# Kernel tuning notes

Measured on AMD Instinct MI355X. Metric: run time of the kernel, lower is better.

## Reference

```python
import jax, jax.numpy as jnp
import numpy as np

N = 6144      # number of pedestrians
HID = 256     # hidden_dim
OUT = 32      # out_dim
NTOP = 4      # n nearest neighbours
EMB = OUT // NTOP  # per-neighbour embedding dim = 8


def setup_inputs() -> dict:
    key = jax.random.key(0)
    ks = jax.random.split(key, 12)
    r = lambda k, shp, s=1.0: (jax.random.normal(k, shp, dtype=jnp.float32) * s)
    return {
        "obs1": r(ks[0], (N, 2)),
        "obs2": r(ks[1], (N, 2)),
        "h": r(ks[2], (N, HID), 0.1),
        "c": r(ks[3], (N, HID), 0.1),
        "W_emb": r(ks[4], (4, EMB), 0.3),
        "b_emb": r(ks[5], (EMB,), 0.1),
        "W_ih": r(ks[6], (4 * HID, OUT), 0.1),
        "b_ih": r(ks[7], (4 * HID,), 0.1),
        "W_hh": r(ks[8], (4 * HID, HID), 0.1),
        "b_hh": r(ks[9], (4 * HID,), 0.1),
        "W_pool": r(ks[10], (OUT, HID), 0.1),
        "b_pool": r(ks[11], (OUT,), 0.1),
    }


def reference(obs1, obs2, h, c, W_emb, b_emb, W_ih, b_ih, W_hh, b_hh, W_pool, b_pool):
    n = obs2.shape[0]
    vel = obs2 - obs1                                   # [N,2]
    # rel_position[i, j] = obs2[j] - obs2[i]
    diff = obs2[None, :, :] - obs2[:, None, :]          # [N,N,2]
    dist = jnp.linalg.norm(diff, axis=-1)               # [N,N]
    # exclude self (torch code drops the diagonal before topk)
    dist = jnp.where(jnp.eye(n, dtype=bool), jnp.inf, dist)
    _, idx = jax.lax.top_k(-dist, NTOP)                 # [N,NTOP] indices of nearest
    nearest_pos = jnp.take_along_axis(diff, idx[:, :, None], axis=1)  # [N,NTOP,2]
    # rel_direction[i, j] = vel[j] - vel[i]
    nearest_vel = vel[idx] - vel[:, None, :]            # [N,NTOP,2]
    feat = jnp.concatenate([nearest_pos, nearest_vel], axis=-1)       # [N,NTOP,4]
    # Linear(4, EMB) + ReLU, then flatten neighbours -> [N, OUT]
    emb = jax.nn.relu(feat @ W_emb + b_emb).reshape(n, -1)
    # LSTMCell (PyTorch gate order: i, f, g, o)
    gates = emb @ W_ih.T + b_ih + h @ W_hh.T + b_hh     # [N,4*HID]
    gi, gf, gg, go = jnp.split(gates, 4, axis=-1)
    c_new = jax.nn.sigmoid(gf) * c + jax.nn.sigmoid(gi) * jnp.tanh(gg)
    h_new = jax.nn.sigmoid(go) * jnp.tanh(c_new)
    out = h_new @ W_pool.T + b_pool                     # [N,OUT]
    return out
```

## Files before the change

### kernel.cpp

```cpp
#include <hip/hip_runtime.h>
#include <math.h>

typedef unsigned short u16;
typedef unsigned long long u64;
typedef __attribute__((ext_vector_type(8))) short bf16x8;
typedef __attribute__((ext_vector_type(4))) float f32x4;

__device__ __forceinline__ float sigf(float x)  { return 1.0f / (1.0f + __expf(-x)); }
__device__ __forceinline__ float tanhf_(float x){ float e = __expf(2.0f * x); return 1.0f - 2.0f / (e + 1.0f); }
__device__ __forceinline__ u16 f2bf(float f) {
    unsigned x = __float_as_uint(f);
    return (u16)((x + 0x7fffu + ((x >> 16) & 1u)) >> 16);
}

#define INSU(KEY) do {                                                              \
    u64 _k = (KEY);                                                                 \
    k3 = (_k < k3) ? _k : k3;                                                       \
    { bool _c = k3 < k2; u64 _lo = _c ? k3 : k2, _hi = _c ? k2 : k3; k2 = _lo; k3 = _hi; } \
    { bool _c = k2 < k1; u64 _lo = _c ? k2 : k1, _hi = _c ? k1 : k2; k1 = _lo; k2 = _hi; } \
    { bool _c = k1 < k0; u64 _lo = _c ? k1 : k0, _hi = _c ? k0 : k1; k0 = _lo; k1 = _hi; } \
} while (0)

#define INS4(D, J) do {                                                              \
    float _d = (D); int _j = (J);                                                    \
    if (_d < bd3 || (_d == bd3 && _j < bj3)) {                                       \
        bd3 = _d; bj3 = _j;                                                          \
        if (bd3 < bd2 || (bd3 == bd2 && bj3 < bj2)) {                                \
            float _t = bd2; bd2 = bd3; bd3 = _t; int _u = bj2; bj2 = bj3; bj3 = _u; }\
        if (bd2 < bd1 || (bd2 == bd1 && bj2 < bj1)) {                                \
            float _t = bd1; bd1 = bd2; bd2 = _t; int _u = bj1; bj1 = bj2; bj2 = _u; }\
        if (bd1 < bd0 || (bd1 == bd0 && bj1 < bj0)) {                                \
            float _t = bd0; bd0 = bd1; bd1 = _t; int _u = bj0; bj0 = bj1; bj1 = _u; }\
    } } while (0)

__global__ void diag_kernel(float* out, int code, int out_size) {
    if (out_size > 0) out[0] = (float)code * 1.0e8f;
}

__device__ __forceinline__ void prep_item(
    int id, const float* Wih, const float* Whh, const float* Wp,
    u16* Wgf, u16* Wpf)
{
    if (id < 36864) {
        int gt = id / 576, rem = id - gt * 576;
        int kt = rem >> 6, ln = rem & 63;
        int g  = gt * 16 + (ln & 15);
        int k  = kt * 32 + (ln >> 4) * 8;
        u16* dst = Wgf + (size_t)id * 8;
        #pragma unroll
        for (int j = 0; j < 8; j++) {
            int kk = k + j;
            float v = (kk < 32) ? Wih[(size_t)g * 32 + kk]
                                : Whh[(size_t)g * 256 + (kk - 32)];
            dst[j] = f2bf(v);
        }
    } else if (id < 37888) {
        int id2 = id - 36864;
        int pt = id2 >> 9, rem = id2 & 511;
        int kt = rem >> 6, ln = rem & 63;
        int o  = pt * 16 + (ln & 15);
        int k  = kt * 32 + (ln >> 4) * 8;
        u16* dst = Wpf + (size_t)id2 * 8;
        #pragma unroll
        for (int j = 0; j < 8; j++)
            dst[j] = f2bf(Wp[(size_t)o * 256 + k + j]);
    }
}

__global__ __launch_bounds__(256) void knn_prep_kernel(
    const float* __restrict__ obs1, const float* __restrict__ obs2,
    const float* __restrict__ Wemb, const float* __restrict__ bemb,
    const float* __restrict__ Wih,  const float* __restrict__ Whh,
    const float* __restrict__ Wp,
    u16* __restrict__ Wgf, u16* __restrict__ Wpf,
    int n, int knn_blocks, float* __restrict__ out)
{
    const int t = threadIdx.x;

    if (blockIdx.x >= knn_blocks) {
        int id = (blockIdx.x - knn_blocks) * 256 + t;
        prep_item(id, Wih, Whh, Wp, Wgf, Wpf);
        return;
    }

    const int lane = t & 63;
    const int wv   = t >> 6;
    const int i    = blockIdx.x * 4 + wv;
    if (i >= n) return;

    const float2* o2 = (const float2*)obs2;
    const float2 pi = o2[i];

    u64 k0 = ~0ull, k1 = ~0ull, k2 = ~0ull, k3 = ~0ull;

    int j = lane;
    for (; j + 192 < n; j += 256) {
        float2 p0 = o2[j], p1 = o2[j + 64], p2 = o2[j + 128], p3 = o2[j + 192];
        float dx, dy, d2; u64 key;
        dx = p0.x - pi.x; dy = p0.y - pi.y;
        d2 = __fadd_rn(__fmul_rn(dx, dx), __fmul_rn(dy, dy));
        key = (((u64)__float_as_uint(d2)) << 24) | (unsigned)j;
        key = (j == i) ? ~0ull : key;                         INSU(key);
        dx = p1.x - pi.x; dy = p1.y - pi.y;
        d2 = __fadd_rn(__fmul_rn(dx, dx), __fmul_rn(dy, dy));
        key = (((u64)__float_as_uint(d2)) << 24) | (unsigned)(j + 64);
        key = (j + 64 == i) ? ~0ull : key;                    INSU(key);
        dx = p2.x - pi.x; dy = p2.y - pi.y;
        d2 = __fadd_rn(__fmul_rn(dx, dx), __fmul_rn(dy, dy));
        key = (((u64)__float_as_uint(d2)) << 24) | (unsigned)(j + 128);
        key = (j + 128 == i) ? ~0ull : key;                   INSU(key);
        dx = p3.x - pi.x; dy = p3.y - pi.y;
        d2 = __fadd_rn(__fmul_rn(dx, dx), __fmul_rn(dy, dy));
        key = (((u64)__float_as_uint(d2)) << 24) | (unsigned)(j + 192);
        key = (j + 192 == i) ? ~0ull : key;                   INSU(key);
    }
    for (; j < n; j += 64) {
        float2 pj = o2[j];
        float dx = pj.x - pi.x, dy = pj.y - pi.y;
        float d2 = __fadd_rn(__fmul_rn(dx, dx), __fmul_rn(dy, dy));
        u64 key = (((u64)__float_as_uint(d2)) << 24) | (unsigned)j;
        key = (j == i) ? ~0ull : key;
        INSU(key);
    }

    #pragma unroll
    for (int m = 1; m < 64; m <<= 1) {
        u64 o0 = __shfl_xor(k0, m), o1 = __shfl_xor(k1, m);
        u64 o2_ = __shfl_xor(k2, m), o3 = __shfl_xor(k3, m);
        INSU(o0); INSU(o1); INSU(o2_); INSU(o3);
    }

    if (lane < 4) {
        u64 kq = (lane == 0) ? k0 : (lane == 1) ? k1 : (lane == 2) ? k2 : k3;
        int jn = (int)(kq & 0xFFFFFF);
        if (jn < 0 || jn >= n) jn = 0;
        float pix = pi.x, piy = pi.y;
        float pjx = obs2[2 * jn], pjy = obs2[2 * jn + 1];
        float px = pjx - pix, py = pjy - piy;
        float vix = pix - obs1[2 * i];
        float viy = piy - obs1[2 * i + 1];
        float vx = (pjx - obs1[2 * jn])     - vix;
        float vy = (pjy - obs1[2 * jn + 1]) - viy;
        float* dst = out + (size_t)i * 32 + lane * 8;
        #pragma unroll
        for (int e = 0; e < 8; e++) {
            float a = px * Wemb[e]      + py * Wemb[8 + e]
                    + vx * Wemb[16 + e] + vy * Wemb[24 + e]
                    + bemb[e];
            dst[e] = fmaxf(a, 0.0f);
        }
    }
}

__global__ __launch_bounds__(512) void lstm_kernel(
    const float* __restrict__ h,   const float* __restrict__ c,
    const u16*  __restrict__ Wgf,  const float* __restrict__ bih,
    const float* __restrict__ bhh,
    const u16*  __restrict__ Wpf,  const float* __restrict__ bp,
    int n, float* __restrict__ out)
{
    __shared__ __align__(16) char lds[17920];
    u16* sXb = (u16*)lds;
    u16* sHb = (u16*)(lds + 9472);

    const int t    = threadIdx.x;
    const int i0   = blockIdx.x * 12;
    const int lane = t & 63;
    const int wv   = t >> 6;
    const int fm   = lane & 15;
    const int fq   = lane >> 4;

    {
        int r = t >> 5, e = t & 31;
        int row = i0 + r;
        float v = (r < 12 && row < n) ? out[(size_t)row * 32 + e] : 0.0f;
        sXb[r * 296 + e] = f2bf(v);
    }
    #pragma unroll
    for (int f = t; f < 16 * 64; f += 512) {
        int r = f >> 6, k4 = f & 63;
        int row = i0 + r;
        float4 hv = (r < 12 && row < n) ? ((const float4*)h)[(size_t)row * 64 + k4]
                                        : make_float4(0.f, 0.f, 0.f, 0.f);
        u16* d = &sXb[r * 296 + 32 + k4 * 4];
        d[0] = f2bf(hv.x); d[1] = f2bf(hv.y); d[2] = f2bf(hv.z); d[3] = f2bf(hv.w);
    }
    __syncthreads();

    bf16x8 afr[9];
    #pragma unroll
    for (int kt = 0; kt < 9; kt++)
        afr[kt] = *(const bf16x8*)&sXb[fm * 296 + kt * 32 + fq * 8];

    #pragma unroll
    for (int ut2 = 0; ut2 < 2; ut2++) {
        const int ut = wv + ut2 * 8;
        const int u  = ut * 16 + fm;

        f32x4 acc[4];
        #pragma unroll
        for (int jg = 0; jg < 4; jg++) acc[jg] = (f32x4){0.f, 0.f, 0.f, 0.f};

        #pragma unroll
        for (int jg = 0; jg < 4; jg++) {
            const int gt = jg * 16 + ut;
            const u16* wbase = Wgf + ((size_t)gt * 9) * 512 + lane * 8;
            #pragma unroll
            for (int kt = 0; kt < 9; kt++) {
                bf16x8 bfr = *(const bf16x8*)(wbase + kt * 512);
                acc[jg] = __builtin_amdgcn_mfma_f32_16x16x32_bf16(afr[kt], bfr, acc[jg], 0, 0, 0);
            }
        }

        float b0 = bih[u]       + bhh[u];
        float b1 = bih[u + 256] + bhh[u + 256];
        float b2 = bih[u + 512] + bhh[u + 512];
        float b3 = bih[u + 768] + bhh[u + 768];

        #pragma unroll
        for (int r_ = 0; r_ < 4; r_++) {
            int rl = fq * 4 + r_;
            int row = i0 + rl;
            bool valid = (rl < 12) && (row < n);
            float cin = valid ? c[(size_t)row * 256 + u] : 0.0f;
            float gi = acc[0][r_] + b0;
            float gf = acc[1][r_] + b1;
            float gg = acc[2][r_] + b2;
            float go = acc[3][r_] + b3;
            float cn = sigf(gf) * cin + sigf(gi) * tanhf_(gg);
            float hn = sigf(go) * tanhf_(cn);
            sHb[rl * 264 + u] = valid ? f2bf(hn) : (u16)0;
        }
    }
    __syncthreads();

    if (wv < 2) {
        bf16x8 ah[8];
        #pragma unroll
        for (int kt = 0; kt < 8; kt++)
            ah[kt] = *(const bf16x8*)&sHb[fm * 264 + kt * 32 + fq * 8];
        const u16* wbase = Wpf + ((size_t)wv * 8) * 512 + lane * 8;
        f32x4 acc = {0.f, 0.f, 0.f, 0.f};
        #pragma unroll
        for (int kt = 0; kt < 8; kt++) {
            bf16x8 bfr = *(const bf16x8*)(wbase + kt * 512);
            acc = __builtin_amdgcn_mfma_f32_16x16x32_bf16(ah[kt], bfr, acc, 0, 0, 0);
        }
        float bias = bp[wv * 16 + fm];
        #pragma unroll
        for (int r_ = 0; r_ < 4; r_++) {
            int rl = fq * 4 + r_;
            int row = i0 + rl;
            if (rl < 12 && row < n) out[(size_t)row * 32 + wv * 16 + fm] = acc[r_] + bias;
        }
    }
}

__global__ __launch_bounds__(256) void nnlstm_fallback(
    const float* __restrict__ obs1, const float* __restrict__ obs2,
    const float* __restrict__ h,    const float* __restrict__ c,
    const float* __restrict__ Wemb, const float* __restrict__ bemb,
    const float* __restrict__ Wih,  const float* __restrict__ bih,
    const float* __restrict__ Whh,  const float* __restrict__ bhh,
    const float* __restrict__ Wp,   const float* __restrict__ bp,
    int n, float* __restrict__ out)
{
    __shared__ float sMd[16][64];
    __shared__ int   sMj[16][64];
    __shared__ float sX[16][292];
    __shared__ float sH[16][264];

    const int t   = threadIdx.x;
    const int sub = t & 15;
    const int ii  = t >> 4;
    const int i0  = blockIdx.x * 16;
    const int i   = i0 + ii;

    for (int v = t; v < 16 * 256; v += 256) {
        int r = v >> 8, k = v & 255;
        int row = i0 + r;
        sX[r][32 + k] = (row < n) ? h[(size_t)row * 256 + k] : 0.0f;
    }

    float bd0 = 1e30f, bd1 = 1e30f, bd2 = 1e30f, bd3 = 1e30f;
    int   bj0 = 0x7fffffff, bj1 = 0x7fffffff, bj2 = 0x7fffffff, bj3 = 0x7fffffff;

    if (i < n) {
        const float pix = obs2[2 * i];
        const float piy = obs2[2 * i + 1];
        for (int j = sub; j < n; j += 16) {
            float dx = obs2[2 * j]     - pix;
            float dy = obs2[2 * j + 1] - piy;
            float d2 = __fadd_rn(__fmul_rn(dx, dx), __fmul_rn(dy, dy));
            float dist = __fsqrt_rn(d2);
            if (j == i) continue;
            INS4(dist, j);
        }
    }
    sMd[ii][sub * 4 + 0] = bd0;  sMj[ii][sub * 4 + 0] = bj0;
    sMd[ii][sub * 4 + 1] = bd1;  sMj[ii][sub * 4 + 1] = bj1;
    sMd[ii][sub * 4 + 2] = bd2;  sMj[ii][sub * 4 + 2] = bj2;
    sMd[ii][sub * 4 + 3] = bd3;  sMj[ii][sub * 4 + 3] = bj3;
    __syncthreads();

    if (t < 16) {
        const int r = t;
        const int irow = i0 + r;
        float bd0 = 1e30f, bd1 = 1e30f, bd2 = 1e30f, bd3 = 1e30f;
        int   bj0 = 0x7fffffff, bj1 = 0x7fffffff, bj2 = 0x7fffffff, bj3 = 0x7fffffff;
        for (int q = 0; q < 64; q++) { INS4(sMd[r][q], sMj[r][q]); }

        if (irow < n) {
            float pix = obs2[2 * irow], piy = obs2[2 * irow + 1];
            float vix = pix - obs1[2 * irow];
            float viy = piy - obs1[2 * irow + 1];
            #pragma unroll
            for (int q2 = 0; q2 < 4; q2++) {
                int jn = (q2 == 0) ? bj0 : (q2 == 1) ? bj1 : (q2 == 2) ? bj2 : bj3;
                if (jn < 0 || jn >= n) jn = 0;
                float pjx = obs2[2 * jn], pjy = obs2[2 * jn + 1];
                float px = pjx - pix, py = pjy - piy;
                float vx = (pjx - obs1[2 * jn])     - vix;
                float vy = (pjy - obs1[2 * jn + 1]) - viy;
                #pragma unroll
                for (int e = 0; e < 8; e++) {
                    float a = px * Wemb[e]      + py * Wemb[8 + e]
                            + vx * Wemb[16 + e] + vy * Wemb[24 + e]
                            + bemb[e];
                    sX[r][q2 * 8 + e] = fmaxf(a, 0.0f);
                }
            }
        } else {
            for (int e = 0; e < 32; e++) sX[r][e] = 0.0f;
        }
    }
    __syncthreads();

    const int uu = t;
    float acc[4][16];
    #pragma unroll
    for (int j = 0; j < 4; j++) {
        float b = bih[uu + 256 * j] + bhh[uu + 256 * j];
        #pragma unroll
        for (int r = 0; r < 16; r++) acc[j][r] = b;
    }

    for (int kc = 0; kc < 288; kc++) {
        float w[4];
        #pragma unroll
        for (int j = 0; j < 4; j++) {
            int g = uu + 256 * j;
            w[j] = (kc < 32) ? Wih[(size_t)g * 32 + kc]
                             : Whh[(size_t)g * 256 + (kc - 32)];
        }
        #pragma unroll
        for (int r = 0; r < 16; r++) {
            float x = sX[r][kc];
            #pragma unroll
            for (int j = 0; j < 4; j++) acc[j][r] += w[j] * x;
        }
    }

    for (int r = 0; r < 16; r++) {
        int row = i0 + r;
        float cin = (row < n) ? c[(size_t)row * 256 + uu] : 0.0f;
        float cn = sigf(acc[1][r]) * cin + sigf(acc[0][r]) * tanhf(acc[2][r]);
        float hn = sigf(acc[3][r]) * tanhf(cn);
        sH[r][uu] = hn;
    }
    __syncthreads();

    for (int v = t; v < 16 * 32; v += 256) {
        int r = v >> 5, o = v & 31;
        int row = i0 + r;
        if (row >= n) continue;
        float a = bp[o];
        for (int kc = 0; kc < 256; kc++)
            a += Wp[(size_t)o * 256 + kc] * sH[r][kc];
        out[(size_t)row * 32 + o] = a;
    }
}

extern "C" void kernel_launch(void* const* d_in, const int* in_sizes, int n_in,
                              void* d_out, int out_size, void* d_ws, size_t ws_size,
                              hipStream_t stream) {
    float* out = (float*)d_out;

    int code = 0, n = 0;
    if (n_in != 12) code = 1;
    else {
        n = in_sizes[1] / 2;
        if (n <= 4 || in_sizes[1] != 2 * n)          code = 2;
        else if (in_sizes[0]  != 2 * n)              code = 3;
        else if (in_sizes[2]  != 256 * n)            code = 4;
        else if (in_sizes[3]  != 256 * n)            code = 5;
        else if (in_sizes[4]  != 32 || in_sizes[5] != 8)        code = 6;
        else if (in_sizes[6]  != 32768 || in_sizes[7] != 1024)  code = 7;
        else if (in_sizes[8]  != 262144 || in_sizes[9] != 1024) code = 8;
        else if (in_sizes[10] != 8192 || in_sizes[11] != 32)    code = 9;
        else if (out_size != 32 * n)                 code = 10;
    }
    if (code != 0) {
        diag_kernel<<<1, 1, 0, stream>>>(out, code, out_size);
        return;
    }

    const float* obs1   = (const float*)d_in[0];
    const float* obs2   = (const float*)d_in[1];
    const float* h      = (const float*)d_in[2];
    const float* c      = (const float*)d_in[3];
    const float* W_emb  = (const float*)d_in[4];
    const float* b_emb  = (const float*)d_in[5];
    const float* W_ih   = (const float*)d_in[6];
    const float* b_ih   = (const float*)d_in[7];
    const float* W_hh   = (const float*)d_in[8];
    const float* b_hh   = (const float*)d_in[9];
    const float* W_pool = (const float*)d_in[10];
    const float* b_pool = (const float*)d_in[11];

    const size_t wgf_bytes = (size_t)36864 * 8 * sizeof(u16);
    const size_t wpf_bytes = (size_t)1024 * 8 * sizeof(u16);

    if (ws_size >= wgf_bytes + wpf_bytes && n <= (1 << 24)) {
        u16* Wgf = (u16*)d_ws;
        u16* Wpf = (u16*)((char*)d_ws + wgf_bytes);
        int knn_blocks = (n + 3) / 4;
        knn_prep_kernel<<<knn_blocks + 148, 256, 0, stream>>>(
            obs1, obs2, W_emb, b_emb, W_ih, W_hh, W_pool, Wgf, Wpf,
            n, knn_blocks, out);
        lstm_kernel<<<(n + 11) / 12, 512, 0, stream>>>(
            h, c, Wgf, b_ih, b_hh, Wpf, b_pool, n, out);
    } else {
        nnlstm_fallback<<<(n + 15) / 16, 256, 0, stream>>>(
            obs1, obs2, h, c, W_emb, b_emb, W_ih, b_ih, W_hh, b_hh,
            W_pool, b_pool, n, out);
    }
}
```

Before: 142.9 us.

## Two-pass KNN: float-only threshold pass, then filtered keyed top-4 selection

Replaces the single pass that ran 64-bit key insertion sorts for every candidate with two passes. The first pass keeps four independent float-only top-4 lists per lane, merges them with min/max networks and a wave butterfly to get the 4th-smallest distance as a threshold. The second pass recomputes distances and does the 64-bit key insert only for candidates at or below that threshold, so most candidates skip it. The cost is reading obs2 and computing distances twice, plus possible lane divergence in the filtered branch.

```diff
diff --git a/kernel.cpp b/kernel.cpp
--- a/kernel.cpp
+++ b/kernel.cpp
@@ -19,6 +19,24 @@
     { bool _c = k3 < k2; u64 _lo = _c ? k3 : k2, _hi = _c ? k2 : k3; k2 = _lo; k3 = _hi; } \
     { bool _c = k2 < k1; u64 _lo = _c ? k2 : k1, _hi = _c ? k1 : k2; k1 = _lo; k2 = _hi; } \
     { bool _c = k1 < k0; u64 _lo = _c ? k1 : k0, _hi = _c ? k0 : k1; k0 = _lo; k1 = _hi; } \
+} while (0)
+
+#define INSF(T0,T1,T2,T3,D) do {                                                    \
+    float _ma = fmaxf((D),(T0)); (T0) = fminf((D),(T0));                            \
+    float _mb = fmaxf(_ma,(T1)); (T1) = fminf(_ma,(T1));                            \
+    float _mc = fmaxf(_mb,(T2)); (T2) = fminf(_mb,(T2));                            \
+    (T3) = fminf(_mc,(T3));                                                         \
+} while (0)
+
+#define MRG4(X0,X1,X2,X3,Y0,Y1,Y2,Y3) do {                                          \
+    float _q0 = fminf((X0),(Y3));                                                   \
+    float _q1 = fminf((X1),(Y2));                                                   \
+    float _q2 = fminf((X2),(Y1));                                                   \
+    float _q3 = fminf((X3),(Y0));                                                   \
+    float _l0 = fminf(_q0,_q2), _h0 = fmaxf(_q0,_q2);                               \
+    float _l1 = fminf(_q1,_q3), _h1 = fmaxf(_q1,_q3);                               \
+    (X0) = fminf(_l0,_l1); (X1) = fmaxf(_l0,_l1);                                   \
+    (X2) = fminf(_h0,_h1); (X3) = fmaxf(_h0,_h1);                                   \
 } while (0)
 
 #define INS4(D, J) do {                                                              \
@@ -88,39 +106,96 @@
     const int i    = blockIdx.x * 4 + wv;
     if (i >= n) return;
 
+    const float FINF = __int_as_float(0x7f800000);
     const float2* o2 = (const float2*)obs2;
     const float2 pi = o2[i];
 
-    u64 k0 = ~0ull, k1 = ~0ull, k2 = ~0ull, k3 = ~0ull;
+    float A0=FINF, A1=FINF, A2=FINF, A3=FINF;
+    float B0=FINF, B1=FINF, B2=FINF, B3=FINF;
+    float C0=FINF, C1=FINF, C2=FINF, C3=FINF;
+    float D0=FINF, D1=FINF, D2=FINF, D3=FINF;
 
     int j = lane;
     for (; j + 192 < n; j += 256) {
         float2 p0 = o2[j], p1 = o2[j + 64], p2 = o2[j + 128], p3 = o2[j + 192];
-        float dx, dy, d2; u64 key;
+        float dx, dy, d2;
         dx = p0.x - pi.x; dy = p0.y - pi.y;
         d2 = __fadd_rn(__fmul_rn(dx, dx), __fmul_rn(dy, dy));
-        key = (((u64)__float_as_uint(d2)) << 24) | (unsigned)j;
-        key = (j == i) ? ~0ull : key;                         INSU(key);
+        d2 = (j == i) ? FINF : d2;               INSF(A0, A1, A2, A3, d2);
         dx = p1.x - pi.x; dy = p1.y - pi.y;
         d2 = __fadd_rn(__fmul_rn(dx, dx), __fmul_rn(dy, dy));
-        key = (((u64)__float_as_uint(d2)) << 24) | (unsigned)(j + 64);
-        key = (j + 64 == i) ? ~0ull : key;                    INSU(key);
+        d2 = (j + 64 == i) ? FINF : d2;          INSF(B0, B1, B2, B3, d2);
         dx = p2.x - pi.x; dy = p2.y - pi.y;
         d2 = __fadd_rn(__fmul_rn(dx, dx), __fmul_rn(dy, dy));
-        key = (((u64)__float_as_uint(d2)) << 24) | (unsigned)(j + 128);
-        key = (j + 128 == i) ? ~0ull : key;                   INSU(key);
+        d2 = (j + 128 == i) ? FINF : d2;         INSF(C0, C1, C2, C3, d2);
         dx = p3.x - pi.x; dy = p3.y - pi.y;
         d2 = __fadd_rn(__fmul_rn(dx, dx), __fmul_rn(dy, dy));
-        key = (((u64)__float_as_uint(d2)) << 24) | (unsigned)(j + 192);
-        key = (j + 192 == i) ? ~0ull : key;                   INSU(key);
+        d2 = (j + 192 == i) ? FINF : d2;         INSF(D0, D1, D2, D3, d2);
     }
     for (; j < n; j += 64) {
         float2 pj = o2[j];
         float dx = pj.x - pi.x, dy = pj.y - pi.y;
         float d2 = __fadd_rn(__fmul_rn(dx, dx), __fmul_rn(dy, dy));
-        u64 key = (((u64)__float_as_uint(d2)) << 24) | (unsigned)j;
-        key = (j == i) ? ~0ull : key;
-        INSU(key);
+        d2 = (j == i) ? FINF : d2;
+        INSF(A0, A1, A2, A3, d2);
+    }
+
+    MRG4(A0, A1, A2, A3, B0, B1, B2, B3);
+    MRG4(C0, C1, C2, C3, D0, D1, D2, D3);
+    MRG4(A0, A1, A2, A3, C0, C1, C2, C3);
+
+    #pragma unroll
+    for (int m = 1; m < 64; m <<= 1) {
+        float y0 = __shfl_xor(A0, m), y1 = __shfl_xor(A1, m);
+        float y2 = __shfl_xor(A2, m), y3 = __shfl_xor(A3, m);
+        MRG4(A0, A1, A2, A3, y0, y1, y2, y3);
+    }
+    const float thr = A3;
+
+    u64 k0 = ~0ull, k1 = ~0ull, k2 = ~0ull, k3 = ~0ull;
+
+    j = lane;
+    for (; j + 192 < n; j += 256) {
+        float2 p0 = o2[j], p1 = o2[j + 64], p2 = o2[j + 128], p3 = o2[j + 192];
+        float dx, dy, d2;
+        dx = p0.x - pi.x; dy = p0.y - pi.y;
+        d2 = __fadd_rn(__fmul_rn(dx, dx), __fmul_rn(dy, dy));
+        if (d2 <= thr) {
+            u64 key = (((u64)__float_as_uint(d2)) << 24) | (unsigned)j;
+            key = (j == i) ? ~0ull : key;
+            INSU(key);
+        }
+        dx = p1.x - pi.x; dy = p1.y - pi.y;
+        d2 = __fadd_rn(__fmul_rn(dx, dx), __fmul_rn(dy, dy));
+        if (d2 <= thr) {
+            u64 key = (((u64)__float_as_uint(d2)) << 24) | (unsigned)(j + 64);
+            key = (j + 64 == i) ? ~0ull : key;
+            INSU(key);
+        }
+        dx = p2.x - pi.x; dy = p2.y - pi.y;
+        d2 = __fadd_rn(__fmul_rn(dx, dx), __fmul_rn(dy, dy));
+        if (d2 <= thr) {
+            u64 key = (((u64)__float_as_uint(d2)) << 24) | (unsigned)(j + 128);
+            key = (j + 128 == i) ? ~0ull : key;
+            INSU(key);
+        }
+        dx = p3.x - pi.x; dy = p3.y - pi.y;
+        d2 = __fadd_rn(__fmul_rn(dx, dx), __fmul_rn(dy, dy));
+        if (d2 <= thr) {
+            u64 key = (((u64)__float_as_uint(d2)) << 24) | (unsigned)(j + 192);
+            key = (j + 192 == i) ? ~0ull : key;
+            INSU(key);
+        }
+    }
+    for (; j < n; j += 64) {
+        float2 pj = o2[j];
+        float dx = pj.x - pi.x, dy = pj.y - pi.y;
+        float d2 = __fadd_rn(__fmul_rn(dx, dx), __fmul_rn(dy, dy));
+        if (d2 <= thr) {
+            u64 key = (((u64)__float_as_uint(d2)) << 24) | (unsigned)j;
+            key = (j == i) ? ~0ull : key;
+            INSU(key);
+        }
     }
 
     #pragma unroll
```

After: 145.7 us. No clear change (+1.9%).

## Two-pass kNN with float threshold pass and LDS-staged positions

Applied to the files above, without the earlier changes.

Splits the nearest-neighbour search into two passes. The first keeps four independent float-only top-4 lists per lane, using min/max networks, and merges them across the wave to get the 4th-smallest distance as a threshold. The second pass does the 64-bit key insertion only for candidates at or below that threshold. For n <= 6144 all positions are also staged in shared memory per block, so both passes read LDS instead of global memory. This trades a second distance sweep and a per-block LDS fill for avoiding the costly 64-bit sorted insert on nearly every candidate.

```diff
diff --git a/kernel.cpp b/kernel.cpp
--- a/kernel.cpp
+++ b/kernel.cpp
@@ -19,6 +19,24 @@
     { bool _c = k3 < k2; u64 _lo = _c ? k3 : k2, _hi = _c ? k2 : k3; k2 = _lo; k3 = _hi; } \
     { bool _c = k2 < k1; u64 _lo = _c ? k2 : k1, _hi = _c ? k1 : k2; k1 = _lo; k2 = _hi; } \
     { bool _c = k1 < k0; u64 _lo = _c ? k1 : k0, _hi = _c ? k0 : k1; k0 = _lo; k1 = _hi; } \
+} while (0)
+
+#define INSF(T0,T1,T2,T3,D) do {                                                    \
+    float _ma = fmaxf((D),(T0)); (T0) = fminf((D),(T0));                            \
+    float _mb = fmaxf(_ma,(T1)); (T1) = fminf(_ma,(T1));                            \
+    float _mc = fmaxf(_mb,(T2)); (T2) = fminf(_mb,(T2));                            \
+    (T3) = fminf(_mc,(T3));                                                         \
+} while (0)
+
+#define MRG4(X0,X1,X2,X3,Y0,Y1,Y2,Y3) do {                                          \
+    float _q0 = fminf((X0),(Y3));                                                   \
+    float _q1 = fminf((X1),(Y2));                                                   \
+    float _q2 = fminf((X2),(Y1));                                                   \
+    float _q3 = fminf((X3),(Y0));                                                   \
+    float _l0 = fminf(_q0,_q2), _h0 = fmaxf(_q0,_q2);                               \
+    float _l1 = fminf(_q1,_q3), _h1 = fmaxf(_q1,_q3);                               \
+    (X0) = fminf(_l0,_l1); (X1) = fmaxf(_l0,_l1);                                   \
+    (X2) = fminf(_h0,_h1); (X3) = fmaxf(_h0,_h1);                                   \
 } while (0)
 
 #define INS4(D, J) do {                                                              \
@@ -67,6 +85,7 @@
     }
 }
 
+template<bool USE_LDS>
 __global__ __launch_bounds__(256) void knn_prep_kernel(
     const float* __restrict__ obs1, const float* __restrict__ obs2,
     const float* __restrict__ Wemb, const float* __restrict__ bemb,
@@ -75,6 +94,9 @@
     u16* __restrict__ Wgf, u16* __restrict__ Wpf,
     int n, int knn_blocks, float* __restrict__ out)
 {
+    extern __shared__ __align__(16) char smem[];
+    float2* sP = (float2*)smem;
+
     const int t = threadIdx.x;
 
     if (blockIdx.x >= knn_blocks) {
@@ -86,42 +108,120 @@
     const int lane = t & 63;
     const int wv   = t >> 6;
     const int i    = blockIdx.x * 4 + wv;
+
+    const float2* o2 = (const float2*)obs2;
+
+    if (USE_LDS) {
+        const float4* o4 = (const float4*)obs2;
+        float4* s4 = (float4*)smem;
+        const int n2 = n >> 1;
+        for (int idx = t; idx < n2; idx += 256) s4[idx] = o4[idx];
+        if ((n & 1) && t == 0) sP[n - 1] = o2[n - 1];
+        __syncthreads();
+    }
+
     if (i >= n) return;
 
-    const float2* o2 = (const float2*)obs2;
+    const float FINF = __int_as_float(0x7f800000);
     const float2 pi = o2[i];
 
+    float A0=FINF, A1=FINF, A2=FINF, A3=FINF;
+    float B0=FINF, B1=FINF, B2=FINF, B3=FINF;
+    float C0=FINF, C1=FINF, C2=FINF, C3=FINF;
+    float D0=FINF, D1=FINF, D2=FINF, D3=FINF;
+
+#define P1LOOP(ARR) do {                                                            \
+    int j = lane;                                                                   \
+    for (; j + 192 < n; j += 256) {                                                 \
+        float2 p0 = (ARR)[j], p1 = (ARR)[j + 64];                                   \
+        float2 p2 = (ARR)[j + 128], p3 = (ARR)[j + 192];                            \
+        float dx, dy, d2;                                                           \
+        dx = p0.x - pi.x; dy = p0.y - pi.y;                                         \
+        d2 = __fadd_rn(__fmul_rn(dx, dx), __fmul_rn(dy, dy));                       \
+        d2 = (j == i) ? FINF : d2;               INSF(A0, A1, A2, A3, d2);          \
+        dx = p1.x - pi.x; dy = p1.y - pi.y;                                         \
+        d2 = __fadd_rn(__fmul_rn(dx, dx), __fmul_rn(dy, dy));                       \
+        d2 = (j + 64 == i) ? FINF : d2;          INSF(B0, B1, B2, B3, d2);          \
+        dx = p2.x - pi.x; dy = p2.y - pi.y;                                         \
+        d2 = __fadd_rn(__fmul_rn(dx, dx), __fmul_rn(dy, dy));                       \
+        d2 = (j + 128 == i) ? FINF : d2;         INSF(C0, C1, C2, C3, d2);          \
+        dx = p3.x - pi.x; dy = p3.y - pi.y;                                         \
+        d2 = __fadd_rn(__fmul_rn(dx, dx), __fmul_rn(dy, dy));                       \
+        d2 = (j + 192 == i) ? FINF : d2;         INSF(D0, D1, D2, D3, d2);          \
+    }                                                                               \
+    for (; j < n; j += 64) {                                                        \
+        float2 pj = (ARR)[j];                                                       \
+        float dx = pj.x - pi.x, dy = pj.y - pi.y;                                   \
+        float d2 = __fadd_rn(__fmul_rn(dx, dx), __fmul_rn(dy, dy));                 \
+        d2 = (j == i) ? FINF : d2;                                                  \
+        INSF(A0, A1, A2, A3, d2);                                                   \
+    }                                                                               \
+} while (0)
+
+    if (USE_LDS) P1LOOP(sP); else P1LOOP(o2);
+
+    MRG4(A0, A1, A2, A3, B0, B1, B2, B3);
+    MRG4(C0, C1, C2, C3, D0, D1, D2, D3);
+    MRG4(A0, A1, A2, A3, C0, C1, C2, C3);
+
+    #pragma unroll
+    for (int m = 1; m < 64; m <<= 1) {
+        float y0 = __shfl_xor(A0, m), y1 = __shfl_xor(A1, m);
+        float y2 = __shfl_xor(A2, m), y3 = __shfl_xor(A3, m);
+        MRG4(A0, A1, A2, A3, y0, y1, y2, y3);
+    }
+    const float thr = A3;
+
     u64 k0 = ~0ull, k1 = ~0ull, k2 = ~0ull, k3 = ~0ull;
 
-    int j = lane;
-    for (; j + 192 < n; j += 256) {
-        float2 p0 = o2[j], p1 = o2[j + 64], p2 = o2[j + 128], p3 = o2[j + 192];
-        float dx, dy, d2; u64 key;
-        dx = p0.x - pi.x; dy = p0.y - pi.y;
-        d2 = __fadd_rn(__fmul_rn(dx, dx), __fmul_rn(dy, dy));
-        key = (((u64)__float_as_uint(d2)) << 24) | (unsigned)j;
-        key = (j == i) ? ~0ull : key;                         INSU(key);
-        dx = p1.x - pi.x; dy = p1.y - pi.y;
-        d2 = __fadd_rn(__fmul_rn(dx, dx), __fmul_rn(dy, dy));
-        key = (((u64)__float_as_uint(d2)) << 24) | (unsigned)(j + 64);
-        key = (j + 64 == i) ? ~0ull : key;                    INSU(key);
-        dx = p2.x - pi.x; dy = p2.y - pi.y;
-        d2 = __fadd_rn(__fmul_rn(dx, dx), __fmul_rn(dy, dy));
-        key = (((u64)__float_as_uint(d2)) << 24) | (unsigned)(j + 128);
-        key = (j + 128 == i) ? ~0ull : key;                   INSU(key);
-        dx = p3.x - pi.x; dy = p3.y - pi.y;
-        d2 = __fadd_rn(__fmul_rn(dx, dx), __fmul_rn(dy, dy));
-        key = (((u64)__float_as_uint(d2)) << 24) | (unsigned)(j + 192);
-        key = (j + 192 == i) ? ~0ull : key;                   INSU(key);
-    }
-    for (; j < n; j += 64) {
-        float2 pj = o2[j];
-        float dx = pj.x - pi.x, dy = pj.y - pi.y;
-        float d2 = __fadd_rn(__fmul_rn(dx, dx), __fmul_rn(dy, dy));
-        u64 key = (((u64)__float_as_uint(d2)) << 24) | (unsigned)j;
-        key = (j == i) ? ~0ull : key;
-        INSU(key);
-    }
+#define P2LOOP(ARR) do {                                                            \
+    int j = lane;                                                                   \
+    for (; j + 192 < n; j += 256) {                                                 \
+        float2 p0 = (ARR)[j], p1 = (ARR)[j + 64];                                   \
+        float2 p2 = (ARR)[j + 128], p3 = (ARR)[j + 192];                            \
+        float dx, dy, d2;                                                           \
+        dx = p0.x - pi.x; dy = p0.y - pi.y;                                         \
+        d2 = __fadd_rn(__fmul_rn(dx, dx), __fmul_rn(dy, dy));                       \
+        if (d2 <= thr) {                                                            \
+            u64 key = (((u64)__float_as_uint(d2)) << 24) | (unsigned)j;             \
+            key = (j == i) ? ~0ull : key;                                           \
+            INSU(key);                                                              \
+        }                                                                           \
+        dx = p1.x - pi.x; dy = p1.y - pi.y;                                         \
+        d2 = __fadd_rn(__fmul_rn(dx, dx), __fmul_rn(dy, dy));                       \
+        if (d2 <= thr) {                                                            \
+            u64 key = (((u64)__float_as_uint(d2)) << 24) | (unsigned)(j + 64);      \
+            key = (j + 64 == i) ? ~0ull : key;                                      \
+            INSU(key);                                                              \
+        }                                                                           \
+        dx = p2.x - pi.x; dy = p2.y - pi.y;                                         \
+        d2 = __fadd_rn(__fmul_rn(dx, dx), __fmul_rn(dy, dy));                       \
+        if (d2 <= thr) {                                                            \
+            u64 key = (((u64)__float_as_uint(d2)) << 24) | (unsigned)(j + 128);     \
+            key = (j + 128 == i) ? ~0ull : key;                                     \
+            INSU(key);                                                              \
+        }                                                                           \
+        dx = p3.x - pi.x; dy = p3.y - pi.y;                                         \
+        d2 = __fadd_rn(__fmul_rn(dx, dx), __fmul_rn(dy, dy));                       \
+        if (d2 <= thr) {                                                            \
+            u64 key = (((u64)__float_as_uint(d2)) << 24) | (unsigned)(j + 192);     \
+            key = (j + 192 == i) ? ~0ull : key;                                     \
+            INSU(key);                                                              \
+        }                                                                           \
+    }                                                                               \
+    for (; j < n; j += 64) {                                                        \
+        float2 pj = (ARR)[j];                                                       \
+        float dx = pj.x - pi.x, dy = pj.y - pi.y;                                   \
+        float d2 = __fadd_rn(__fmul_rn(dx, dx), __fmul_rn(dy, dy));                 \
+        if (d2 <= thr) {                                                            \
+            u64 key = (((u64)__float_as_uint(d2)) << 24) | (unsigned)j;             \
+            key = (j == i) ? ~0ull : key;                                           \
+            INSU(key);                                                              \
+        }                                                                           \
+    }                                                                               \
+} while (0)
+
+    if (USE_LDS) P2LOOP(sP); else P2LOOP(o2);
 
     #pragma unroll
     for (int m = 1; m < 64; m <<= 1) {
@@ -425,9 +525,16 @@
         u16* Wgf = (u16*)d_ws;
         u16* Wpf = (u16*)((char*)d_ws + wgf_bytes);
         int knn_blocks = (n + 3) / 4;
-        knn_prep_kernel<<<knn_blocks + 148, 256, 0, stream>>>(
-            obs1, obs2, W_emb, b_emb, W_ih, W_hh, W_pool, Wgf, Wpf,
-            n, knn_blocks, out);
+        if (n <= 6144) {
+            size_t shmem = (size_t)n * sizeof(float2);
+            knn_prep_kernel<true><<<knn_blocks + 148, 256, shmem, stream>>>(
+                obs1, obs2, W_emb, b_emb, W_ih, W_hh, W_pool, Wgf, Wpf,
+                n, knn_blocks, out);
+        } else {
+            knn_prep_kernel<false><<<knn_blocks + 148, 256, 0, stream>>>(
+                obs1, obs2, W_emb, b_emb, W_ih, W_hh, W_pool, Wgf, Wpf,
+                n, knn_blocks, out);
+        }
         lstm_kernel<<<(n + 11) / 12, 512, 0, stream>>>(
             h, c, Wgf, b_ih, b_hh, Wpf, b_pool, n, out);
     } else {
```

After: 142.9 us. No clear change (-0.0%).

## Two-pass KNN: cheap min-distance threshold pass, then filtered top-4 insertion

Applied to the files above, without the earlier changes.

The KNN search now runs a first pass that keeps only per-lane minimum distances, merges them across the wavefront with a bitonic-style 4-way merge, and takes the 4th smallest of the lane minima as a threshold. A second pass recomputes distances and only does the costly 64-bit sorted insertion for candidates at or under that threshold. This cuts the comparator-network work per candidate at the cost of reading obs2 twice. The weight prep also switches to float4 loads, and launch bounds gain a min-blocks hint.

```diff
diff --git a/kernel.cpp b/kernel.cpp
--- a/kernel.cpp
+++ b/kernel.cpp
@@ -19,6 +19,17 @@
     { bool _c = k3 < k2; u64 _lo = _c ? k3 : k2, _hi = _c ? k2 : k3; k2 = _lo; k3 = _hi; } \
     { bool _c = k2 < k1; u64 _lo = _c ? k2 : k1, _hi = _c ? k1 : k2; k1 = _lo; k2 = _hi; } \
     { bool _c = k1 < k0; u64 _lo = _c ? k1 : k0, _hi = _c ? k0 : k1; k0 = _lo; k1 = _hi; } \
+} while (0)
+
+#define MRG4(X0,X1,X2,X3,Y0,Y1,Y2,Y3) do {                                          \
+    float _q0 = fminf((X0),(Y3));                                                   \
+    float _q1 = fminf((X1),(Y2));                                                   \
+    float _q2 = fminf((X2),(Y1));                                                   \
+    float _q3 = fminf((X3),(Y0));                                                   \
+    float _l0 = fminf(_q0,_q2), _h0 = fmaxf(_q0,_q2);                               \
+    float _l1 = fminf(_q1,_q3), _h1 = fmaxf(_q1,_q3);                               \
+    (X0) = fminf(_l0,_l1); (X1) = fmaxf(_l0,_l1);                                   \
+    (X2) = fminf(_h0,_h1); (X3) = fmaxf(_h0,_h1);                                   \
 } while (0)
 
 #define INS4(D, J) do {                                                              \
@@ -47,13 +58,12 @@
         int g  = gt * 16 + (ln & 15);
         int k  = kt * 32 + (ln >> 4) * 8;
         u16* dst = Wgf + (size_t)id * 8;
-        #pragma unroll
-        for (int j = 0; j < 8; j++) {
-            int kk = k + j;
-            float v = (kk < 32) ? Wih[(size_t)g * 32 + kk]
-                                : Whh[(size_t)g * 256 + (kk - 32)];
-            dst[j] = f2bf(v);
-        }
+        const float* src = (k < 32) ? (Wih + (size_t)g * 32 + k)
+                                    : (Whh + (size_t)g * 256 + (k - 32));
+        float4 v0 = ((const float4*)src)[0];
+        float4 v1 = ((const float4*)src)[1];
+        dst[0] = f2bf(v0.x); dst[1] = f2bf(v0.y); dst[2] = f2bf(v0.z); dst[3] = f2bf(v0.w);
+        dst[4] = f2bf(v1.x); dst[5] = f2bf(v1.y); dst[6] = f2bf(v1.z); dst[7] = f2bf(v1.w);
     } else if (id < 37888) {
         int id2 = id - 36864;
         int pt = id2 >> 9, rem = id2 & 511;
@@ -61,13 +71,15 @@
         int o  = pt * 16 + (ln & 15);
         int k  = kt * 32 + (ln >> 4) * 8;
         u16* dst = Wpf + (size_t)id2 * 8;
-        #pragma unroll
-        for (int j = 0; j < 8; j++)
-            dst[j] = f2bf(Wp[(size_t)o * 256 + k + j]);
-    }
-}
-
-__global__ __launch_bounds__(256) void knn_prep_kernel(
+        const float* src = Wp + (size_t)o * 256 + k;
+        float4 v0 = ((const float4*)src)[0];
+        float4 v1 = ((const float4*)src)[1];
+        dst[0] = f2bf(v0.x); dst[1] = f2bf(v0.y); dst[2] = f2bf(v0.z); dst[3] = f2bf(v0.w);
+        dst[4] = f2bf(v1.x); dst[5] = f2bf(v1.y); dst[6] = f2bf(v1.z); dst[7] = f2bf(v1.w);
+    }
+}
+
+__global__ __launch_bounds__(256, 4) void knn_prep_kernel(
     const float* __restrict__ obs1, const float* __restrict__ obs2,
     const float* __restrict__ Wemb, const float* __restrict__ bemb,
     const float* __restrict__ Wih,  const float* __restrict__ Whh,
@@ -88,39 +100,73 @@
     const int i    = blockIdx.x * 4 + wv;
     if (i >= n) return;
 
+    const float FINF = __int_as_float(0x7f800000);
     const float2* o2 = (const float2*)obs2;
     const float2 pi = o2[i];
 
-    u64 k0 = ~0ull, k1 = ~0ull, k2 = ~0ull, k3 = ~0ull;
+    float mm[8];
+    #pragma unroll
+    for (int q = 0; q < 8; q++) mm[q] = FINF;
 
     int j = lane;
-    for (; j + 192 < n; j += 256) {
-        float2 p0 = o2[j], p1 = o2[j + 64], p2 = o2[j + 128], p3 = o2[j + 192];
-        float dx, dy, d2; u64 key;
-        dx = p0.x - pi.x; dy = p0.y - pi.y;
-        d2 = __fadd_rn(__fmul_rn(dx, dx), __fmul_rn(dy, dy));
-        key = (((u64)__float_as_uint(d2)) << 24) | (unsigned)j;
-        key = (j == i) ? ~0ull : key;                         INSU(key);
-        dx = p1.x - pi.x; dy = p1.y - pi.y;
-        d2 = __fadd_rn(__fmul_rn(dx, dx), __fmul_rn(dy, dy));
-        key = (((u64)__float_as_uint(d2)) << 24) | (unsigned)(j + 64);
-        key = (j + 64 == i) ? ~0ull : key;                    INSU(key);
-        dx = p2.x - pi.x; dy = p2.y - pi.y;
-        d2 = __fadd_rn(__fmul_rn(dx, dx), __fmul_rn(dy, dy));
-        key = (((u64)__float_as_uint(d2)) << 24) | (unsigned)(j + 128);
-        key = (j + 128 == i) ? ~0ull : key;                   INSU(key);
-        dx = p3.x - pi.x; dy = p3.y - pi.y;
-        d2 = __fadd_rn(__fmul_rn(dx, dx), __fmul_rn(dy, dy));
-        key = (((u64)__float_as_uint(d2)) << 24) | (unsigned)(j + 192);
-        key = (j + 192 == i) ? ~0ull : key;                   INSU(key);
+    for (; j + 960 < n; j += 1024) {
+        float2 p[16];
+        #pragma unroll
+        for (int q = 0; q < 16; q++) p[q] = o2[j + q * 64];
+        #pragma unroll
+        for (int q = 0; q < 16; q++) {
+            float dx = p[q].x - pi.x, dy = p[q].y - pi.y;
+            float d2 = __fadd_rn(__fmul_rn(dx, dx), __fmul_rn(dy, dy));
+            d2 = (j + q * 64 == i) ? FINF : d2;
+            mm[q & 7] = fminf(mm[q & 7], d2);
+        }
     }
     for (; j < n; j += 64) {
         float2 pj = o2[j];
         float dx = pj.x - pi.x, dy = pj.y - pi.y;
         float d2 = __fadd_rn(__fmul_rn(dx, dx), __fmul_rn(dy, dy));
-        u64 key = (((u64)__float_as_uint(d2)) << 24) | (unsigned)j;
-        key = (j == i) ? ~0ull : key;
-        INSU(key);
+        d2 = (j == i) ? FINF : d2;
+        mm[0] = fminf(mm[0], d2);
+    }
+    const float mn = fminf(fminf(fminf(mm[0], mm[1]), fminf(mm[2], mm[3])),
+                           fminf(fminf(mm[4], mm[5]), fminf(mm[6], mm[7])));
+
+    float A0 = mn, A1 = FINF, A2 = FINF, A3 = FINF;
+    #pragma unroll
+    for (int m = 1; m < 64; m <<= 1) {
+        float y0 = __shfl_xor(A0, m), y1 = __shfl_xor(A1, m);
+        float y2 = __shfl_xor(A2, m), y3 = __shfl_xor(A3, m);
+        MRG4(A0, A1, A2, A3, y0, y1, y2, y3);
+    }
+    const float thr = A3;
+
+    u64 k0 = ~0ull, k1 = ~0ull, k2 = ~0ull, k3 = ~0ull;
+
+    j = lane;
+    for (; j + 448 < n; j += 512) {
+        float2 p[8];
+        #pragma unroll
+        for (int q = 0; q < 8; q++) p[q] = o2[j + q * 64];
+        #pragma unroll
+        for (int q = 0; q < 8; q++) {
+            float dx = p[q].x - pi.x, dy = p[q].y - pi.y;
+            float d2 = __fadd_rn(__fmul_rn(dx, dx), __fmul_rn(dy, dy));
+            if (d2 <= thr) {
+                u64 key = (((u64)__float_as_uint(d2)) << 24) | (unsigned)(j + q * 64);
+                key = (j + q * 64 == i) ? ~0ull : key;
+                INSU(key);
+            }
+        }
+    }
+    for (; j < n; j += 64) {
+        float2 pj = o2[j];
+        float dx = pj.x - pi.x, dy = pj.y - pi.y;
+        float d2 = __fadd_rn(__fmul_rn(dx, dx), __fmul_rn(dy, dy));
+        if (d2 <= thr) {
+            u64 key = (((u64)__float_as_uint(d2)) << 24) | (unsigned)j;
+            key = (j == i) ? ~0ull : key;
+            INSU(key);
+        }
     }
 
     #pragma unroll
```

Measured after the change: 141.9 us. About the same (-0.7%).
